# Performance work log

Measured on AMD Instinct MI355X. Metric: run time of the kernel, lower is better.

Reference implementation:

```python
import jax, jax.numpy as jnp
import numpy as np
import math

B, S, D, H = 4, 2048, 1024, 16
HD = D // H  # 64


def setup_inputs() -> dict:
    key = jax.random.key(0)
    ks = jax.random.split(key, 12)
    s_in = 1.0 / math.sqrt(D)
    inp = {
        "x_v": jax.random.normal(ks[0], (B, S, D), jnp.float32),
        "x_k": jax.random.normal(ks[1], (B, S, D), jnp.float32),
        "x_q": jax.random.normal(ks[2], (B, S, D), jnp.float32),
        "mask": jax.random.randint(ks[3], (B, S, S), 0, 2, jnp.int32),
        "Wq": jax.random.normal(ks[4], (H, D, HD), jnp.float32) * s_in,
        "bq": jax.random.normal(ks[5], (H, HD), jnp.float32) * s_in,
        "Wk": jax.random.normal(ks[6], (H, D, HD), jnp.float32) * s_in,
        "bk": jax.random.normal(ks[7], (H, HD), jnp.float32) * s_in,
        "Wv": jax.random.normal(ks[8], (H, D, HD), jnp.float32) * s_in,
        "bv": jax.random.normal(ks[9], (H, HD), jnp.float32) * s_in,
        "Wo": jax.random.normal(ks[10], (D, D), jnp.float32) * s_in,
        "bo": jax.random.normal(ks[11], (D,), jnp.float32) * s_in,
    }
    return inp


def reference(x_v, x_k, x_q, mask, Wq, bq, Wk, bk, Wv, bv, Wo, bo):
    # Batched per-head projections: [B,S,D] x [H,D,E] -> [B,H,S,E]
    q = jnp.einsum("bsd,hde->bhse", x_q, Wq) + bq[None, :, None, :]
    k = jnp.einsum("bsd,hde->bhse", x_k, Wk) + bk[None, :, None, :]
    v = jnp.einsum("bsd,hde->bhse", x_v, Wv) + bv[None, :, None, :]
    scale = 1.0 / math.sqrt(HD)
    scores = jnp.einsum("bhqe,bhke->bhqk", q, k) * scale  # [B,H,Sq,Sk]
    # Faithful to original: masked positions are set to 0 (not -inf) BEFORE softmax
    scores = jnp.where(mask[:, None, :, :] == 0, 0.0, scores)
    attn = jax.nn.softmax(scores, axis=-1)
    z = jnp.einsum("bhqk,bhke->bhqe", attn, v)  # [B,H,Sq,E]
    # Concat over heads in head order (matches torch.cat along dim=2)
    z = z.transpose(0, 2, 1, 3).reshape(B, S, D)
    return z @ Wo + bo
```

## Files before the change

### kernel.cpp

```cpp
#include <hip/hip_runtime.h>

typedef unsigned short u16;
typedef unsigned long long u64;
typedef __attribute__((ext_vector_type(8))) short bf16x8;
typedef __attribute__((ext_vector_type(4))) float f32x4;

#define C_SCALE 0.18033688011112043f

__device__ __forceinline__ u16 f2b(float x) {
  union { float f; unsigned u; } c; c.f = x;
  unsigned r = (c.u + 0x7fffu + ((c.u >> 16) & 1u)) >> 16;
  return (u16)r;
}

__device__ __forceinline__ unsigned pk2(float a, float b) {
#if __has_builtin(__builtin_amdgcn_cvt_pk_bf16_f32)
  typedef __attribute__((ext_vector_type(2))) __bf16 b2;
  b2 r = __builtin_amdgcn_cvt_pk_bf16_f32(a, b);
  union { b2 v; unsigned u; } c; c.v = r;
  return c.u;
#else
  union { float f; unsigned u; } x, y;
  x.f = a; y.f = b;
  return ((x.u + 0x8000u) >> 16) | ((y.u + 0x8000u) & 0xffff0000u);
#endif
}

__device__ __forceinline__ float blo(int w) {
  union { int i; float f; } c; c.i = w << 16; return c.f;
}
__device__ __forceinline__ float bhi(int w) {
  union { int i; float f; } c; c.i = w & 0xffff0000; return c.f;
}

__device__ __forceinline__ void gll16(const u16* g, u16* l) {
  __builtin_amdgcn_global_load_lds(
      (const __attribute__((address_space(1))) void*)g,
      (__attribute__((address_space(3))) void*)l, 16, 0, 0);
}

__global__ __launch_bounds__(256) void cvt_bf16_3(
    const float4* __restrict__ s0, const float4* __restrict__ s1,
    const float4* __restrict__ s2, ushort4* __restrict__ d0,
    ushort4* __restrict__ d1, ushort4* __restrict__ d2, int n4) {
  const int z = blockIdx.y;
  const float4* src = z == 0 ? s0 : z == 1 ? s1 : s2;
  ushort4* dst = z == 0 ? d0 : z == 1 ? d1 : d2;
  int stride = gridDim.x * 256;
  for (int i = blockIdx.x * 256 + threadIdx.x; i < n4; i += stride) {
    float4 v = src[i];
    ushort4 o = { f2b(v.x), f2b(v.y), f2b(v.z), f2b(v.w) };
    dst[i] = o;
  }
}

__global__ __launch_bounds__(256) void transpose_cvt_all(
    const float* __restrict__ Wq, const float* __restrict__ Wk,
    const float* __restrict__ Wv, const float* __restrict__ Wo,
    u16* __restrict__ wq_t, u16* __restrict__ wk_t,
    u16* __restrict__ wv_t, u16* __restrict__ wo_t) {
  __shared__ u16 tile[64][65];
  const int id = blockIdx.x;
  const int which = id >> 8, sub = id & 255;
  const float* s;
  u16* d;
  int R, C, r0, c0;
  if (which < 3) {
    const float* W = which == 0 ? Wq : which == 1 ? Wk : Wv;
    u16* D = which == 0 ? wq_t : which == 1 ? wk_t : wv_t;
    int h = sub >> 4, rt = sub & 15;
    s = W + (size_t)h * 1024 * 64;
    d = D + (size_t)h * 64 * 1024;
    R = 1024; C = 64; r0 = rt * 64; c0 = 0;
  } else {
    s = Wo; d = wo_t;
    R = 1024; C = 1024; r0 = ((sub >> 4) & 15) * 64; c0 = (sub & 15) * 64;
  }
  const int t = threadIdx.x;
#pragma unroll
  for (int rep = 0; rep < 16; ++rep) {
    int idx = rep * 256 + t;
    int i = idx >> 6, j = idx & 63;
    tile[j][i] = f2b(s[(size_t)(r0 + i) * C + c0 + j]);
  }
  __syncthreads();
#pragma unroll
  for (int rep = 0; rep < 16; ++rep) {
    int idx = rep * 256 + t;
    int jj = idx >> 6, ii = idx & 63;
    d[(size_t)(c0 + jj) * R + r0 + ii] = tile[jj][ii];
  }
}

__global__ __launch_bounds__(256) void expand_mask(
    const int4* __restrict__ m, ushort4* __restrict__ mb, int n4) {
  int stride = gridDim.x * 256;
  for (int i = blockIdx.x * 256 + threadIdx.x; i < n4; i += stride) {
    int4 v = m[i];
    ushort4 o = { (u16)(v.x ? 0x3f80 : 0), (u16)(v.y ? 0x3f80 : 0),
                  (u16)(v.z ? 0x3f80 : 0), (u16)(v.w ? 0x3f80 : 0) };
    mb[i] = o;
  }
}

__device__ __forceinline__ void gemm_core(
    const u16* __restrict__ A, const u16* __restrict__ W,
    u16* Asm, u16* Bsm, int s0, int n0, int wv, int lane,
    int m16, int q4, f32x4 acc[4][4]) {
  const int rsub = lane >> 3, csub = lane & 7;
  const int wr = (wv & 1) * 64, wc = (wv >> 1) * 64;
  for (int k0 = 0; k0 < 1024; k0 += 64) {
    __syncthreads();
#pragma unroll
    for (int i = 0; i < 4; ++i) {
      int chunk = wv * 4 + i;
      gll16(A + (size_t)(s0 + chunk * 8 + rsub) * 1024 + k0 + csub * 8,
            Asm + chunk * 512 + lane * 8);
      gll16(W + (size_t)(n0 + chunk * 8 + rsub) * 1024 + k0 + csub * 8,
            Bsm + chunk * 512 + lane * 8);
    }
    __syncthreads();
#pragma unroll
    for (int ks = 0; ks < 2; ++ks) {
      bf16x8 af[4], bfr[4];
#pragma unroll
      for (int i = 0; i < 4; ++i)
        af[i] = *(const bf16x8*)(Asm + (wr + i * 16 + m16) * 64 + ks * 32 + q4 * 8);
#pragma unroll
      for (int j = 0; j < 4; ++j)
        bfr[j] = *(const bf16x8*)(Bsm + (wc + j * 16 + m16) * 64 + ks * 32 + q4 * 8);
#pragma unroll
      for (int i = 0; i < 4; ++i)
#pragma unroll
        for (int j = 0; j < 4; ++j)
          acc[i][j] = __builtin_amdgcn_mfma_f32_16x16x32_bf16(af[i], bfr[j], acc[i][j], 0, 0, 0);
    }
  }
}

__global__ __launch_bounds__(256, 3) void qkv_gemm(
    const u16* __restrict__ xq, const u16* __restrict__ xk,
    const u16* __restrict__ xv, const u16* __restrict__ wq,
    const u16* __restrict__ wk, const u16* __restrict__ wv_,
    const float* __restrict__ bq, const float* __restrict__ bk,
    const float* __restrict__ bv, u16* __restrict__ qb,
    u16* __restrict__ kb, u16* __restrict__ vtb) {
  __shared__ u16 S[17408];
  u16* Asm = S;
  u16* Bsm = S + 8192;
  const int z = blockIdx.z;
  const u16* A = z == 0 ? xq : z == 1 ? xk : xv;
  const u16* W = z == 0 ? wq : z == 1 ? wk : wv_;
  const float* bias = z == 0 ? bq : z == 1 ? bk : bv;
  const int s0 = blockIdx.x * 128, n0 = blockIdx.y * 128;
  const int t = threadIdx.x, wvi = t >> 6, lane = t & 63;
  const int m16 = lane & 15, q4 = lane >> 4;
  const int wr = (wvi & 1) * 64, wc = (wvi >> 1) * 64;
  f32x4 acc[4][4];
#pragma unroll
  for (int i = 0; i < 4; ++i)
#pragma unroll
    for (int j = 0; j < 4; ++j) acc[i][j] = (f32x4){0.f, 0.f, 0.f, 0.f};

  gemm_core(A, W, Asm, Bsm, s0, n0, wvi, lane, m16, q4, acc);

  if (z < 2) {
    u16* out = z == 0 ? qb : kb;
    const float scale = z == 0 ? C_SCALE : 1.0f;
#pragma unroll
    for (int j = 0; j < 4; ++j) {
      int n = n0 + wc + j * 16 + m16;
      int h = n >> 6, e = n & 63;
      float bval = bias[n];
#pragma unroll
      for (int i = 0; i < 4; ++i)
#pragma unroll
        for (int r = 0; r < 4; ++r) {
          int s = s0 + wr + i * 16 + q4 * 4 + r;
          int bi = s >> 11, sl = s & 2047;
          out[((size_t)(bi * 16 + h) * 2048 + sl) * 64 + e] =
              f2b((acc[i][j][r] + bval) * scale);
        }
    }
  } else {
    __syncthreads();
#pragma unroll
    for (int j = 0; j < 4; ++j) {
      int nl = wc + j * 16 + m16;
      float bval = bias[n0 + nl];
#pragma unroll
      for (int i = 0; i < 4; ++i)
#pragma unroll
        for (int r = 0; r < 4; ++r)
          S[nl * 136 + wr + i * 16 + q4 * 4 + r] = f2b(acc[i][j][r] + bval);
    }
    __syncthreads();
    const int bi = s0 >> 11, sl0 = s0 & 2047;
#pragma unroll
    for (int rep = 0; rep < 8; ++rep) {
      int u = rep * 256 + t;
      int rr = u >> 4, cc = (u & 15) * 8;
      int n = n0 + rr, h = n >> 6, e = n & 63;
      *(int4*)(vtb + ((size_t)(bi * 16 + h) * 64 + e) * 2048 + sl0 + cc) =
          *(const int4*)(S + rr * 136 + cc);
    }
  }
}

__global__ __launch_bounds__(256, 2) void out_gemm(
    const u16* __restrict__ Z, const u16* __restrict__ Wot,
    const float* __restrict__ bo, float* __restrict__ out) {
  __shared__ u16 S[17408];
  u16* Asm = S;
  u16* Bsm = S + 8192;
  const int s0 = blockIdx.x * 128, n0 = blockIdx.y * 128;
  const int t = threadIdx.x, wvi = t >> 6, lane = t & 63;
  const int m16 = lane & 15, q4 = lane >> 4;
  const int wr = (wvi & 1) * 64, wc = (wvi >> 1) * 64;
  f32x4 acc[4][4];
#pragma unroll
  for (int i = 0; i < 4; ++i)
#pragma unroll
    for (int j = 0; j < 4; ++j) acc[i][j] = (f32x4){0.f, 0.f, 0.f, 0.f};

  gemm_core(Z, Wot, Asm, Bsm, s0, n0, wvi, lane, m16, q4, acc);

#pragma unroll
  for (int j = 0; j < 4; ++j) {
    int n = n0 + wc + j * 16 + m16;
    float bval = bo[n];
#pragma unroll
    for (int i = 0; i < 4; ++i)
#pragma unroll
      for (int r = 0; r < 4; ++r) {
        int s = s0 + wr + i * 16 + q4 * 4 + r;
        out[(size_t)s * 1024 + n] = acc[i][j][r] + bval;
      }
  }
}

__global__ __launch_bounds__(512, 4) void attn(
    const u16* __restrict__ qb, const u16* __restrict__ kb,
    const u16* __restrict__ vt, const u16* __restrict__ mk,
    u16* __restrict__ zb) {
  __shared__ u16 Kl[2][4096];
  __shared__ u16 Vl[2][4096];
  const int id = blockIdx.x;
  const int qi = id >> 6;
  const int bh = id & 63;
  const int b = bh >> 4, h = bh & 15;
  const int t = threadIdx.x, w = t >> 6, lane = t & 63;
  const int m16 = lane & 15, q4 = lane >> 4;
  const size_t bho = (size_t)bh * 2048;
  const u16* qp = qb + bho * 64;
  const u16* kp = kb + bho * 64;
  const u16* vp = vt + bho * 64;
  const int qbase = qi * 256 + w * 32;

  bf16x8 qa[2][2];
#pragma unroll
  for (int qg = 0; qg < 2; ++qg)
#pragma unroll
    for (int ks = 0; ks < 2; ++ks)
      qa[qg][ks] = *(const bf16x8*)(qp + (size_t)(qbase + qg * 16 + m16) * 64 + ks * 32 + q4 * 8);

  f32x4 oacc[2][4], lacc[2];
#pragma unroll
  for (int qg = 0; qg < 2; ++qg) {
    lacc[qg] = (f32x4){0.f, 0.f, 0.f, 0.f};
#pragma unroll
    for (int g = 0; g < 4; ++g) oacc[qg][g] = (f32x4){0.f, 0.f, 0.f, 0.f};
  }
  bf16x8 ones;
#pragma unroll
  for (int j = 0; j < 8; ++j) ones[j] = (short)0x3f80;

  const u16* mrow[2];
  mrow[0] = mk + ((size_t)b * 2048 + qbase + m16) * 2048;
  mrow[1] = mk + ((size_t)b * 2048 + qbase + 16 + m16) * 2048;

  const int ch = t & 7, rw = t >> 3;
  const int r5 = rw & 31;
  const int sK = (rw & 32) + (((r5 >> 2) & 1) * 16) + (((r5 >> 3) & 3) * 4) + (r5 & 3);

  const int kwc = (ch ^ (sK & 7)) * 8;
  const int vwc = (ch ^ (rw & 7)) * 8;
  const int sw = (m16 & 7) * 8;
  const int rcol0 = (q4 * 8) ^ sw;
  const int rcol1 = (32 + q4 * 8) ^ sw;

  int4 pk0 = *(const int4*)(kp + (size_t)rw * 64 + ch * 8);
  int4 pv0 = *(const int4*)(vp + (size_t)rw * 2048 + ch * 8);
  int4 cm[2][2], nm[2][2];
#pragma unroll
  for (int qg = 0; qg < 2; ++qg)
#pragma unroll
    for (int bb = 0; bb < 2; ++bb)
      cm[qg][bb] = *(const int4*)(mrow[qg] + bb * 32 + q4 * 8);
  *(int4*)(&Kl[0][sK * 64 + kwc]) = pk0;
  *(int4*)(&Vl[0][rw * 64 + vwc]) = pv0;
  __syncthreads();

  for (int kt = 0; kt < 32; ++kt) {
    const int cur = kt & 1;
    if (kt < 31) {
      const int k0n = (kt + 1) * 64;
      pk0 = *(const int4*)(kp + (size_t)(k0n + rw) * 64 + ch * 8);
      pv0 = *(const int4*)(vp + (size_t)rw * 2048 + k0n + ch * 8);
#pragma unroll
      for (int qg = 0; qg < 2; ++qg)
#pragma unroll
        for (int bb = 0; bb < 2; ++bb)
          nm[qg][bb] = *(const int4*)(mrow[qg] + k0n + bb * 32 + q4 * 8);
    }

#pragma unroll
    for (int bb = 0; bb < 2; ++bb) {
      const int rb = bb * 32;
      const int vc = bb ? rcol1 : rcol0;
      bf16x8 kf00 = *(const bf16x8*)(&Kl[cur][(rb + m16) * 64 + rcol0]);
      bf16x8 kf01 = *(const bf16x8*)(&Kl[cur][(rb + m16) * 64 + rcol1]);
      bf16x8 kf10 = *(const bf16x8*)(&Kl[cur][(rb + 16 + m16) * 64 + rcol0]);
      bf16x8 kf11 = *(const bf16x8*)(&Kl[cur][(rb + 16 + m16) * 64 + rcol1]);
      bf16x8 pa[2];
#pragma unroll
      for (int qg = 0; qg < 2; ++qg) {
        f32x4 sa = (f32x4){0.f, 0.f, 0.f, 0.f};
        f32x4 sb = (f32x4){0.f, 0.f, 0.f, 0.f};
        sa = __builtin_amdgcn_mfma_f32_16x16x32_bf16(kf00, qa[qg][0], sa, 0, 0, 0);
        sa = __builtin_amdgcn_mfma_f32_16x16x32_bf16(kf01, qa[qg][1], sa, 0, 0, 0);
        sb = __builtin_amdgcn_mfma_f32_16x16x32_bf16(kf10, qa[qg][0], sb, 0, 0, 0);
        sb = __builtin_amdgcn_mfma_f32_16x16x32_bf16(kf11, qa[qg][1], sb, 0, 0, 0);
        const int4 mw = cm[qg][bb];
        float p[8];
        p[0] = __builtin_amdgcn_exp2f(sa[0] * blo(mw.x));
        p[1] = __builtin_amdgcn_exp2f(sa[1] * bhi(mw.x));
        p[2] = __builtin_amdgcn_exp2f(sa[2] * blo(mw.y));
        p[3] = __builtin_amdgcn_exp2f(sa[3] * bhi(mw.y));
        p[4] = __builtin_amdgcn_exp2f(sb[0] * blo(mw.z));
        p[5] = __builtin_amdgcn_exp2f(sb[1] * bhi(mw.z));
        p[6] = __builtin_amdgcn_exp2f(sb[2] * blo(mw.w));
        p[7] = __builtin_amdgcn_exp2f(sb[3] * bhi(mw.w));
        union { unsigned u[4]; bf16x8 v; } pu;
        pu.u[0] = pk2(p[0], p[1]);
        pu.u[1] = pk2(p[2], p[3]);
        pu.u[2] = pk2(p[4], p[5]);
        pu.u[3] = pk2(p[6], p[7]);
        pa[qg] = pu.v;
        lacc[qg] = __builtin_amdgcn_mfma_f32_16x16x32_bf16(pa[qg], ones, lacc[qg], 0, 0, 0);
      }
#pragma unroll
      for (int e = 0; e < 4; ++e) {
        bf16x8 vf = *(const bf16x8*)(&Vl[cur][(e * 16 + m16) * 64 + vc]);
        oacc[0][e] = __builtin_amdgcn_mfma_f32_16x16x32_bf16(pa[0], vf, oacc[0][e], 0, 0, 0);
        oacc[1][e] = __builtin_amdgcn_mfma_f32_16x16x32_bf16(pa[1], vf, oacc[1][e], 0, 0, 0);
      }
    }

    if (kt < 31) {
      const int nxt = cur ^ 1;
      *(int4*)(&Kl[nxt][sK * 64 + kwc]) = pk0;
      *(int4*)(&Vl[nxt][rw * 64 + vwc]) = pv0;
#pragma unroll
      for (int qg = 0; qg < 2; ++qg)
#pragma unroll
        for (int bb = 0; bb < 2; ++bb) cm[qg][bb] = nm[qg][bb];
      __syncthreads();
    }
  }

#pragma unroll
  for (int qg = 0; qg < 2; ++qg) {
#pragma unroll
    for (int r = 0; r < 4; ++r) {
      float inv = __builtin_amdgcn_rcpf(lacc[qg][r]);
      size_t zr = ((size_t)b * 2048 + qbase + qg * 16 + q4 * 4 + r) * 1024 + h * 64;
#pragma unroll
      for (int e = 0; e < 4; ++e) {
        zb[zr + e * 16 + m16] = f2b(oacc[qg][e][r] * inv);
      }
    }
  }
}

extern "C" void kernel_launch(void* const* d_in, const int* in_sizes, int n_in,
                              void* d_out, int out_size, void* d_ws, size_t ws_size,
                              hipStream_t stream) {
  const float* x_v = (const float*)d_in[0];
  const float* x_k = (const float*)d_in[1];
  const float* x_q = (const float*)d_in[2];
  const int* mask = (const int*)d_in[3];
  const float* Wq = (const float*)d_in[4];
  const float* bq = (const float*)d_in[5];
  const float* Wk = (const float*)d_in[6];
  const float* bk = (const float*)d_in[7];
  const float* Wv = (const float*)d_in[8];
  const float* bv = (const float*)d_in[9];
  const float* Wo = (const float*)d_in[10];
  const float* bo = (const float*)d_in[11];
  float* out = (float*)d_out;

  char* ws = (char*)d_ws;
  size_t off = 0;
  auto alloc_u16 = [&](size_t n) {
    u16* p = (u16*)(ws + off);
    off += n * sizeof(u16);
    return p;
  };
  u16* wq_t = alloc_u16((size_t)16 * 64 * 1024);
  u16* wk_t = alloc_u16((size_t)16 * 64 * 1024);
  u16* wv_t = alloc_u16((size_t)16 * 64 * 1024);
  u16* wo_t = alloc_u16((size_t)1024 * 1024);
  u16* qb = alloc_u16((size_t)8192 * 1024);
  u16* kb = alloc_u16((size_t)8192 * 1024);
  u16* vtb = alloc_u16((size_t)8192 * 1024);
  u16* xq16 = alloc_u16((size_t)8192 * 1024);
  u16* xk16 = alloc_u16((size_t)8192 * 1024);
  u16* xv16 = alloc_u16((size_t)8192 * 1024);
  u16* zb = xq16;
  u16* mask16 = xk16;

  transpose_cvt_all<<<dim3(1024), 256, 0, stream>>>(
      Wq, Wk, Wv, Wo, wq_t, wk_t, wv_t, wo_t);
  const int n4 = 8192 * 1024 / 4;
  cvt_bf16_3<<<dim3(512, 3), 256, 0, stream>>>(
      (const float4*)x_q, (const float4*)x_k, (const float4*)x_v,
      (ushort4*)xq16, (ushort4*)xk16, (ushort4*)xv16, n4);
  qkv_gemm<<<dim3(64, 8, 3), 256, 0, stream>>>(
      xq16, xk16, xv16, wq_t, wk_t, wv_t, bq, bk, bv, qb, kb, vtb);
  expand_mask<<<dim3(2048), 256, 0, stream>>>(
      (const int4*)mask, (ushort4*)mask16, 4 * 2048 * 2048 / 4);
  attn<<<dim3(512), 512, 0, stream>>>(qb, kb, vtb, mask16, zb);
  out_gemm<<<dim3(64, 8), 256, 0, stream>>>(zb, wo_t, bo, out);
}
```

Before: 394.7 us.

## Unroll attention K-loop by two and apply the mask by bit-select after exp

```diff
diff --git a/kernel.cpp b/kernel.cpp
--- a/kernel.cpp
+++ b/kernel.cpp
@@ -24,13 +24,6 @@
   x.f = a; y.f = b;
   return ((x.u + 0x8000u) >> 16) | ((y.u + 0x8000u) & 0xffff0000u);
 #endif
-}
-
-__device__ __forceinline__ float blo(int w) {
-  union { int i; float f; } c; c.i = w << 16; return c.f;
-}
-__device__ __forceinline__ float bhi(int w) {
-  union { int i; float f; } c; c.i = w & 0xffff0000; return c.f;
 }
 
 __device__ __forceinline__ void gll16(const u16* g, u16* l) {
@@ -97,8 +90,8 @@
   int stride = gridDim.x * 256;
   for (int i = blockIdx.x * 256 + threadIdx.x; i < n4; i += stride) {
     int4 v = m[i];
-    ushort4 o = { (u16)(v.x ? 0x3f80 : 0), (u16)(v.y ? 0x3f80 : 0),
-                  (u16)(v.z ? 0x3f80 : 0), (u16)(v.w ? 0x3f80 : 0) };
+    ushort4 o = { (u16)(v.x ? 0xFFFF : 0), (u16)(v.y ? 0xFFFF : 0),
+                  (u16)(v.z ? 0xFFFF : 0), (u16)(v.w ? 0xFFFF : 0) };
     mb[i] = o;
   }
 }
@@ -239,6 +232,94 @@
   }
 }
 
+#define PBLEND(PA, SA, SB, MW) do {                                         \
+    float p0_ = __builtin_amdgcn_exp2f((SA)[0]);                            \
+    float p1_ = __builtin_amdgcn_exp2f((SA)[1]);                            \
+    float p2_ = __builtin_amdgcn_exp2f((SA)[2]);                            \
+    float p3_ = __builtin_amdgcn_exp2f((SA)[3]);                            \
+    float p4_ = __builtin_amdgcn_exp2f((SB)[0]);                            \
+    float p5_ = __builtin_amdgcn_exp2f((SB)[1]);                            \
+    float p6_ = __builtin_amdgcn_exp2f((SB)[2]);                            \
+    float p7_ = __builtin_amdgcn_exp2f((SB)[3]);                            \
+    unsigned m0_ = (unsigned)(MW).x, m1_ = (unsigned)(MW).y;                \
+    unsigned m2_ = (unsigned)(MW).z, m3_ = (unsigned)(MW).w;                \
+    union { unsigned u[4]; bf16x8 v; } pu_;                                 \
+    pu_.u[0] = (m0_ & pk2(p0_, p1_)) | (~m0_ & 0x3f803f80u);                \
+    pu_.u[1] = (m1_ & pk2(p2_, p3_)) | (~m1_ & 0x3f803f80u);                \
+    pu_.u[2] = (m2_ & pk2(p4_, p5_)) | (~m2_ & 0x3f803f80u);                \
+    pu_.u[3] = (m3_ & pk2(p6_, p7_)) | (~m3_ & 0x3f803f80u);                \
+    PA = pu_.v;                                                             \
+  } while (0)
+
+#define ATTN_TILE(BUF, M00, M01, M10, M11) do {                             \
+    {                                 \
+      bf16x8 kf00 = *(const bf16x8*)(&Kl[BUF][(m16) * 64 + rcol0]);         \
+      bf16x8 kf01 = *(const bf16x8*)(&Kl[BUF][(m16) * 64 + rcol1]);         \
+      bf16x8 kf10 = *(const bf16x8*)(&Kl[BUF][(16 + m16) * 64 + rcol0]);    \
+      bf16x8 kf11 = *(const bf16x8*)(&Kl[BUF][(16 + m16) * 64 + rcol1]);    \
+      bf16x8 pa0, pa1;                                                      \
+      {                                                                     \
+        f32x4 sa = (f32x4){0.f, 0.f, 0.f, 0.f};                             \
+        f32x4 sb = (f32x4){0.f, 0.f, 0.f, 0.f};                             \
+        sa = __builtin_amdgcn_mfma_f32_16x16x32_bf16(kf00, qa[0][0], sa, 0, 0, 0); \
+        sa = __builtin_amdgcn_mfma_f32_16x16x32_bf16(kf01, qa[0][1], sa, 0, 0, 0); \
+        sb = __builtin_amdgcn_mfma_f32_16x16x32_bf16(kf10, qa[0][0], sb, 0, 0, 0); \
+        sb = __builtin_amdgcn_mfma_f32_16x16x32_bf16(kf11, qa[0][1], sb, 0, 0, 0); \
+        PBLEND(pa0, sa, sb, M00);                                           \
+        lacc[0] = __builtin_amdgcn_mfma_f32_16x16x32_bf16(pa0, ones, lacc[0], 0, 0, 0); \
+      }                                                                     \
+      {                                                                     \
+        f32x4 sa = (f32x4){0.f, 0.f, 0.f, 0.f};                             \
+        f32x4 sb = (f32x4){0.f, 0.f, 0.f, 0.f};                             \
+        sa = __builtin_amdgcn_mfma_f32_16x16x32_bf16(kf00, qa[1][0], sa, 0, 0, 0); \
+        sa = __builtin_amdgcn_mfma_f32_16x16x32_bf16(kf01, qa[1][1], sa, 0, 0, 0); \
+        sb = __builtin_amdgcn_mfma_f32_16x16x32_bf16(kf10, qa[1][0], sb, 0, 0, 0); \
+        sb = __builtin_amdgcn_mfma_f32_16x16x32_bf16(kf11, qa[1][1], sb, 0, 0, 0); \
+        PBLEND(pa1, sa, sb, M10);                                           \
+        lacc[1] = __builtin_amdgcn_mfma_f32_16x16x32_bf16(pa1, ones, lacc[1], 0, 0, 0); \
+      }                                                                     \
+      _Pragma("unroll")                                                     \
+      for (int e = 0; e < 4; ++e) {                                         \
+        bf16x8 vf = *(const bf16x8*)(&Vl[BUF][(e * 16 + m16) * 64 + rcol0]);\
+        oacc[0][e] = __builtin_amdgcn_mfma_f32_16x16x32_bf16(pa0, vf, oacc[0][e], 0, 0, 0); \
+        oacc[1][e] = __builtin_amdgcn_mfma_f32_16x16x32_bf16(pa1, vf, oacc[1][e], 0, 0, 0); \
+      }                                                                     \
+    }                                                                       \
+    {                                \
+      bf16x8 kf00 = *(const bf16x8*)(&Kl[BUF][(32 + m16) * 64 + rcol0]);    \
+      bf16x8 kf01 = *(const bf16x8*)(&Kl[BUF][(32 + m16) * 64 + rcol1]);    \
+      bf16x8 kf10 = *(const bf16x8*)(&Kl[BUF][(48 + m16) * 64 + rcol0]);    \
+      bf16x8 kf11 = *(const bf16x8*)(&Kl[BUF][(48 + m16) * 64 + rcol1]);    \
+      bf16x8 pa0, pa1;                                                      \
+      {                                                                     \
+        f32x4 sa = (f32x4){0.f, 0.f, 0.f, 0.f};                             \
+        f32x4 sb = (f32x4){0.f, 0.f, 0.f, 0.f};                             \
+        sa = __builtin_amdgcn_mfma_f32_16x16x32_bf16(kf00, qa[0][0], sa, 0, 0, 0); \
+        sa = __builtin_amdgcn_mfma_f32_16x16x32_bf16(kf01, qa[0][1], sa, 0, 0, 0); \
+        sb = __builtin_amdgcn_mfma_f32_16x16x32_bf16(kf10, qa[0][0], sb, 0, 0, 0); \
+        sb = __builtin_amdgcn_mfma_f32_16x16x32_bf16(kf11, qa[0][1], sb, 0, 0, 0); \
+        PBLEND(pa0, sa, sb, M01);                                           \
+        lacc[0] = __builtin_amdgcn_mfma_f32_16x16x32_bf16(pa0, ones, lacc[0], 0, 0, 0); \
+      }                                                                     \
+      {                                                                     \
+        f32x4 sa = (f32x4){0.f, 0.f, 0.f, 0.f};                             \
+        f32x4 sb = (f32x4){0.f, 0.f, 0.f, 0.f};                             \
+        sa = __builtin_amdgcn_mfma_f32_16x16x32_bf16(kf00, qa[1][0], sa, 0, 0, 0); \
+        sa = __builtin_amdgcn_mfma_f32_16x16x32_bf16(kf01, qa[1][1], sa, 0, 0, 0); \
+        sb = __builtin_amdgcn_mfma_f32_16x16x32_bf16(kf10, qa[1][0], sb, 0, 0, 0); \
+        sb = __builtin_amdgcn_mfma_f32_16x16x32_bf16(kf11, qa[1][1], sb, 0, 0, 0); \
+        PBLEND(pa1, sa, sb, M11);                                           \
+        lacc[1] = __builtin_amdgcn_mfma_f32_16x16x32_bf16(pa1, ones, lacc[1], 0, 0, 0); \
+      }                                                                     \
+      _Pragma("unroll")                                                     \
+      for (int e = 0; e < 4; ++e) {                                         \
+        bf16x8 vf = *(const bf16x8*)(&Vl[BUF][(e * 16 + m16) * 64 + rcol1]);\
+        oacc[0][e] = __builtin_amdgcn_mfma_f32_16x16x32_bf16(pa0, vf, oacc[0][e], 0, 0, 0); \
+        oacc[1][e] = __builtin_amdgcn_mfma_f32_16x16x32_bf16(pa1, vf, oacc[1][e], 0, 0, 0); \
+      }                                                                     \
+    }                                                                       \
+  } while (0)
+
 __global__ __launch_bounds__(512, 4) void attn(
     const u16* __restrict__ qb, const u16* __restrict__ kb,
     const u16* __restrict__ vt, const u16* __restrict__ mk,
@@ -275,9 +356,8 @@
 #pragma unroll
   for (int j = 0; j < 8; ++j) ones[j] = (short)0x3f80;
 
-  const u16* mrow[2];
-  mrow[0] = mk + ((size_t)b * 2048 + qbase + m16) * 2048;
-  mrow[1] = mk + ((size_t)b * 2048 + qbase + 16 + m16) * 2048;
+  const u16* mrow0 = mk + ((size_t)b * 2048 + qbase + m16) * 2048;
+  const u16* mrow1 = mrow0 + (size_t)16 * 2048;
 
   const int ch = t & 7, rw = t >> 3;
   const int r5 = rw & 31;
@@ -291,80 +371,43 @@
 
   int4 pk0 = *(const int4*)(kp + (size_t)rw * 64 + ch * 8);
   int4 pv0 = *(const int4*)(vp + (size_t)rw * 2048 + ch * 8);
-  int4 cm[2][2], nm[2][2];
-#pragma unroll
-  for (int qg = 0; qg < 2; ++qg)
-#pragma unroll
-    for (int bb = 0; bb < 2; ++bb)
-      cm[qg][bb] = *(const int4*)(mrow[qg] + bb * 32 + q4 * 8);
+  int4 a00 = *(const int4*)(mrow0 + q4 * 8);
+  int4 a01 = *(const int4*)(mrow0 + 32 + q4 * 8);
+  int4 a10 = *(const int4*)(mrow1 + q4 * 8);
+  int4 a11 = *(const int4*)(mrow1 + 32 + q4 * 8);
+  int4 b00, b01, b10, b11;
   *(int4*)(&Kl[0][sK * 64 + kwc]) = pk0;
   *(int4*)(&Vl[0][rw * 64 + vwc]) = pv0;
   __syncthreads();
 
-  for (int kt = 0; kt < 32; ++kt) {
-    const int cur = kt & 1;
-    if (kt < 31) {
-      const int k0n = (kt + 1) * 64;
-      pk0 = *(const int4*)(kp + (size_t)(k0n + rw) * 64 + ch * 8);
-      pv0 = *(const int4*)(vp + (size_t)rw * 2048 + k0n + ch * 8);
-#pragma unroll
-      for (int qg = 0; qg < 2; ++qg)
-#pragma unroll
-        for (int bb = 0; bb < 2; ++bb)
-          nm[qg][bb] = *(const int4*)(mrow[qg] + k0n + bb * 32 + q4 * 8);
-    }
-
-#pragma unroll
-    for (int bb = 0; bb < 2; ++bb) {
-      const int rb = bb * 32;
-      const int vc = bb ? rcol1 : rcol0;
-      bf16x8 kf00 = *(const bf16x8*)(&Kl[cur][(rb + m16) * 64 + rcol0]);
-      bf16x8 kf01 = *(const bf16x8*)(&Kl[cur][(rb + m16) * 64 + rcol1]);
-      bf16x8 kf10 = *(const bf16x8*)(&Kl[cur][(rb + 16 + m16) * 64 + rcol0]);
-      bf16x8 kf11 = *(const bf16x8*)(&Kl[cur][(rb + 16 + m16) * 64 + rcol1]);
-      bf16x8 pa[2];
-#pragma unroll
-      for (int qg = 0; qg < 2; ++qg) {
-        f32x4 sa = (f32x4){0.f, 0.f, 0.f, 0.f};
-        f32x4 sb = (f32x4){0.f, 0.f, 0.f, 0.f};
-        sa = __builtin_amdgcn_mfma_f32_16x16x32_bf16(kf00, qa[qg][0], sa, 0, 0, 0);
-        sa = __builtin_amdgcn_mfma_f32_16x16x32_bf16(kf01, qa[qg][1], sa, 0, 0, 0);
-        sb = __builtin_amdgcn_mfma_f32_16x16x32_bf16(kf10, qa[qg][0], sb, 0, 0, 0);
-        sb = __builtin_amdgcn_mfma_f32_16x16x32_bf16(kf11, qa[qg][1], sb, 0, 0, 0);
-        const int4 mw = cm[qg][bb];
-        float p[8];
-        p[0] = __builtin_amdgcn_exp2f(sa[0] * blo(mw.x));
-        p[1] = __builtin_amdgcn_exp2f(sa[1] * bhi(mw.x));
-        p[2] = __builtin_amdgcn_exp2f(sa[2] * blo(mw.y));
-        p[3] = __builtin_amdgcn_exp2f(sa[3] * bhi(mw.y));
-        p[4] = __builtin_amdgcn_exp2f(sb[0] * blo(mw.z));
-        p[5] = __builtin_amdgcn_exp2f(sb[1] * bhi(mw.z));
-        p[6] = __builtin_amdgcn_exp2f(sb[2] * blo(mw.w));
-        p[7] = __builtin_amdgcn_exp2f(sb[3] * bhi(mw.w));
-        union { unsigned u[4]; bf16x8 v; } pu;
-        pu.u[0] = pk2(p[0], p[1]);
-        pu.u[1] = pk2(p[2], p[3]);
-        pu.u[2] = pk2(p[4], p[5]);
-        pu.u[3] = pk2(p[6], p[7]);
-        pa[qg] = pu.v;
-        lacc[qg] = __builtin_amdgcn_mfma_f32_16x16x32_bf16(pa[qg], ones, lacc[qg], 0, 0, 0);
-      }
-#pragma unroll
-      for (int e = 0; e < 4; ++e) {
-        bf16x8 vf = *(const bf16x8*)(&Vl[cur][(e * 16 + m16) * 64 + vc]);
-        oacc[0][e] = __builtin_amdgcn_mfma_f32_16x16x32_bf16(pa[0], vf, oacc[0][e], 0, 0, 0);
-        oacc[1][e] = __builtin_amdgcn_mfma_f32_16x16x32_bf16(pa[1], vf, oacc[1][e], 0, 0, 0);
-      }
-    }
-
-    if (kt < 31) {
-      const int nxt = cur ^ 1;
-      *(int4*)(&Kl[nxt][sK * 64 + kwc]) = pk0;
-      *(int4*)(&Vl[nxt][rw * 64 + vwc]) = pv0;
-#pragma unroll
-      for (int qg = 0; qg < 2; ++qg)
-#pragma unroll
-        for (int bb = 0; bb < 2; ++bb) cm[qg][bb] = nm[qg][bb];
+  for (int kt = 0; kt < 32; kt += 2) {
+    {
+      const int k1 = (kt + 1) * 64;
+      pk0 = *(const int4*)(kp + (size_t)(k1 + rw) * 64 + ch * 8);
+      pv0 = *(const int4*)(vp + (size_t)rw * 2048 + k1 + ch * 8);
+      b00 = *(const int4*)(mrow0 + k1 + q4 * 8);
+      b01 = *(const int4*)(mrow0 + k1 + 32 + q4 * 8);
+      b10 = *(const int4*)(mrow1 + k1 + q4 * 8);
+      b11 = *(const int4*)(mrow1 + k1 + 32 + q4 * 8);
+    }
+    ATTN_TILE(0, a00, a01, a10, a11);
+    *(int4*)(&Kl[1][sK * 64 + kwc]) = pk0;
+    *(int4*)(&Vl[1][rw * 64 + vwc]) = pv0;
+    __syncthreads();
+
+    if (kt < 30) {
+      const int k2 = (kt + 2) * 64;
+      pk0 = *(const int4*)(kp + (size_t)(k2 + rw) * 64 + ch * 8);
+      pv0 = *(const int4*)(vp + (size_t)rw * 2048 + k2 + ch * 8);
+      a00 = *(const int4*)(mrow0 + k2 + q4 * 8);
+      a01 = *(const int4*)(mrow0 + k2 + 32 + q4 * 8);
+      a10 = *(const int4*)(mrow1 + k2 + q4 * 8);
+      a11 = *(const int4*)(mrow1 + k2 + 32 + q4 * 8);
+    }
+    ATTN_TILE(1, b00, b01, b10, b11);
+    if (kt < 30) {
+      *(int4*)(&Kl[0][sK * 64 + kwc]) = pk0;
+      *(int4*)(&Vl[0][rw * 64 + vwc]) = pv0;
       __syncthreads();
     }
   }
```

Result: slower. 429.5 us (+8.8%).
